# Optimization experiments

Measured on AMD Instinct MI355X. Metric: run time of the kernel, lower is better.

The kernel has to match this reference:

```python
import jax, jax.numpy as jnp
import numpy as np

B, D, AED = 64, 1024, 64
DM = D + AED          # d_model = 1088
H = 8                 # heads, head_dim = 136
DFF = 2048
L = 2                 # encoder layers
R = 487               # reference set size -> total seq = 512
EPS = 1e-5


def setup_inputs() -> dict:
    key = jax.random.key(0)
    ks = jax.random.split(key, 24)
    s = 0.02
    return {
        "query_embedding": jax.random.normal(ks[0], (B, 1, D), jnp.float32),
        "supportActives_embedding": jax.random.normal(ks[1], (B, 12, D), jnp.float32),
        "supportInactives_embedding": jax.random.normal(ks[2], (B, 12, D), jnp.float32),
        "supportSetActivesSize": jax.random.randint(ks[3], (B,), 0, 13, jnp.int64 if jax.config.jax_enable_x64 else jnp.int32),
        "supportSetInactivesSize": jax.random.randint(ks[4], (B,), 0, 13, jnp.int64 if jax.config.jax_enable_x64 else jnp.int32),
        "referenceSet": jax.random.normal(ks[5], (B, R, D), jnp.float32),
        # stacked per-layer params (PyTorch TransformerEncoderLayer, post-norm, relu)
        "Wqkv": jax.random.normal(ks[6], (L, 3 * DM, DM), jnp.float32) * s,
        "bqkv": jnp.zeros((L, 3 * DM), jnp.float32),
        "Wo": jax.random.normal(ks[7], (L, DM, DM), jnp.float32) * s,
        "bo": jnp.zeros((L, DM), jnp.float32),
        "ln1_w": jnp.ones((L, DM), jnp.float32),
        "ln1_b": jnp.zeros((L, DM), jnp.float32),
        "W1": jax.random.normal(ks[8], (L, DFF, DM), jnp.float32) * s,
        "b1": jnp.zeros((L, DFF), jnp.float32),
        "W2": jax.random.normal(ks[9], (L, DM, DFF), jnp.float32) * s,
        "b2": jnp.zeros((L, DM), jnp.float32),
        "ln2_w": jnp.ones((L, DM), jnp.float32),
        "ln2_b": jnp.zeros((L, DM), jnp.float32),
    }


def _ln(x, w, b):
    mu = jnp.mean(x, axis=-1, keepdims=True)
    var = jnp.mean(jnp.square(x - mu), axis=-1, keepdims=True)
    return (x - mu) * jax.lax.rsqrt(var + EPS) * w + b


def _encoder(S, key_pad_mask, Wqkv, bqkv, Wo, bo, ln1_w, ln1_b, W1, b1, W2, b2, ln2_w, ln2_b):
    # key_pad_mask: [B, Sn] bool, True = masked OUT (PyTorch semantics)
    Bn, Sn, _ = S.shape
    hd = DM // H
    bias = jnp.where(key_pad_mask[:, None, None, :], jnp.float32(-1e9), jnp.float32(0.0))
    x = S
    for l in range(L):
        qkv = x @ Wqkv[l].T + bqkv[l]                       # [B,S,3*DM]
        q, k, v = jnp.split(qkv, 3, axis=-1)
        q = q.reshape(Bn, Sn, H, hd)
        k = k.reshape(Bn, Sn, H, hd)
        v = v.reshape(Bn, Sn, H, hd)
        scores = jnp.einsum("bqhd,bkhd->bhqk", q, k) / jnp.sqrt(jnp.float32(hd))
        attn = jax.nn.softmax(scores + bias, axis=-1)
        o = jnp.einsum("bhqk,bkhd->bqhd", attn, v).reshape(Bn, Sn, DM)
        o = o @ Wo[l].T + bo[l]
        x = _ln(x + o, ln1_w[l], ln1_b[l])                  # post-norm
        h = jax.nn.relu(x @ W1[l].T + b1[l])
        x = _ln(x + (h @ W2[l].T + b2[l]), ln2_w[l], ln2_b[l])
    return x


def reference(query_embedding, supportActives_embedding, supportInactives_embedding,
              supportSetActivesSize, supportSetInactivesSize, referenceSet,
              Wqkv, bqkv, Wo, bo, ln1_w, ln1_b, W1, b1, W2, b2, ln2_w, ln2_b):
    Dh = supportActives_embedding.shape[2]
    pad0 = lambda x: jnp.concatenate([x, jnp.zeros_like(x[:, :, :AED])], axis=2)
    q = pad0(query_embedding)
    ref = pad0(referenceSet)
    sa = jnp.concatenate([supportActives_embedding, jnp.ones_like(supportActives_embedding[:, :, :AED])], axis=2)
    si = jnp.concatenate([supportInactives_embedding, -jnp.ones_like(supportInactives_embedding[:, :, :AED])], axis=2)
    S = jnp.concatenate([q, sa, si, ref], axis=1)           # [B, 1+12+12+R, DM]
    Sn = S.shape[1]
    j = jnp.arange(Sn)[None, :]
    ra = supportSetActivesSize[:, None]
    ri = supportSetInactivesSize[:, None]
    # vectorized replica of the double loop; True = mask out (PyTorch semantics)
    mask = (j == 0) | ((j >= 1) & (j < 13) & (j < ra + 1)) | ((j >= 13) & (j < 25) & (j < ri + 13)) | ((j >= 25) & (j < ri + 13))
    S = _encoder(S, mask, Wqkv, bqkv, Wo, bo, ln1_w, ln1_b, W1, b1, W2, b2, ln2_w, ln2_b)
    q_out = S[:, 0:1, :Dh]
    sa_out = S[:, 1:13, :Dh]
    si_out = S[:, 13:25, :Dh]
    return (q_out, sa_out, si_out)
```

## Files before the change

kernel.cpp:

```cpp
#include <hip/hip_runtime.h>

typedef unsigned short u16;
typedef unsigned int u32;
typedef __attribute__((ext_vector_type(8))) short short8;
typedef __attribute__((ext_vector_type(4))) float f32x4;

#define B_ 64
#define D_ 1024
#define DM_ 1088
#define H_ 8
#define HD_ 136
#define DFF_ 2048
#define SN_ 512
#define DM3_ 3264

__device__ __forceinline__ u16 f2bf(float f) {
    union { float f; u32 u; } v; v.f = f;
    u32 r = v.u + 0x7FFFu + ((v.u >> 16) & 1u);
    return (u16)(r >> 16);
}
__device__ __forceinline__ float bf2f(u16 u) {
    union { u32 u; float f; } v; v.u = (u32)u << 16; return v.f;
}

__device__ __forceinline__ void gload16(const void* g, void* l) {
    __builtin_amdgcn_global_load_lds(
        (const __attribute__((address_space(1))) u32*)g,
        (__attribute__((address_space(3))) u32*)l, 16, 0, 0);
}

__global__ void cvt_bf16(const float* __restrict__ in, u16* __restrict__ out, int n) {
    int i = blockIdx.x * 256 + threadIdx.x;
    if (i < n) out[i] = f2bf(in[i]);
}

__global__ void build_s(const float* __restrict__ qe, const float* __restrict__ sa,
                        const float* __restrict__ si, const float* __restrict__ ref,
                        u16* __restrict__ xb) {
    int idx = blockIdx.x * 256 + threadIdx.x;
    const int total = B_ * SN_ * (DM_ / 4);
    if (idx >= total) return;
    int b = idx / (SN_ * 272);
    int rem = idx - b * (SN_ * 272);
    int j = rem / 272;
    int c4 = rem - j * 272;
    int col = c4 * 4;
    float4 v;
    if (col < D_) {
        const float* src;
        if (j == 0)       src = qe + (size_t)b * D_;
        else if (j < 13)  src = sa + ((size_t)b * 12 + (j - 1)) * D_;
        else if (j < 25)  src = si + ((size_t)b * 12 + (j - 13)) * D_;
        else              src = ref + ((size_t)b * 487 + (j - 25)) * D_;
        v = *(const float4*)(src + col);
    } else {
        float f = (j >= 1 && j < 13) ? 1.f : ((j >= 13 && j < 25) ? -1.f : 0.f);
        v = make_float4(f, f, f, f);
    }
    size_t off = ((size_t)b * SN_ + j) * DM_ + col;
    ushort4 p; p.x = f2bf(v.x); p.y = f2bf(v.y); p.z = f2bf(v.z); p.w = f2bf(v.w);
    *(ushort4*)(xb + off) = p;
}

__global__ void build_mask(const int* __restrict__ asz, const int* __restrict__ isz,
                           float* __restrict__ mb) {
    int idx = blockIdx.x * 256 + threadIdx.x;
    if (idx >= B_ * SN_) return;
    int b = idx >> 9, j = idx & 511;
    int ra = asz[b], ri = isz[b];
    bool m = (j == 0) || (j >= 1 && j < 13 && j < ra + 1)
          || (j >= 13 && j < 25 && j < ri + 13) || (j >= 25 && j < ri + 13);
    mb[idx] = m ? -1e9f : 0.f;
}

template<int EPI>
__global__ __launch_bounds__(512, 2)
void gemm256(const u16* __restrict__ A, int lda, const u16* __restrict__ Bt,
             const float* __restrict__ bias, u16* __restrict__ C,
             int N, int K, int nbx) {
    __shared__ __align__(16) u16 As3[3][256 * 32];
    __shared__ __align__(16) u16 Bs3[3][256 * 32];
    const int tid = threadIdx.x;
    const int lane = tid & 63;
    const int l16 = lane & 15;
    const int lhi = lane >> 4;
    const int wave = tid >> 6;
    const int arow = (wave >> 2) * 128;
    const int bcol = (wave & 3) * 64;

    const int nwg = gridDim.x;
    const int cpx = nwg >> 3;
    const int bid = blockIdx.x;
    const int swz = (bid & 7) * cpx + (bid >> 3);
    const int by = swz / nbx;
    const int bx = swz - by * nbx;
    const int bm = by * 256;
    const int bn = bx * 256;

    auto STAGE = [&](int buf, int kt) {
        const int k0 = kt << 5;
        u16* as = As3[buf];
        u16* bs = Bs3[buf];
        #pragma unroll
        for (int p = 0; p < 2; ++p) {
            int c = p * 512 + tid;
            int row = c >> 2;
            int slot = (c & 3) ^ ((row >> 1) & 3);
            gload16(A + (size_t)(bm + row) * lda + k0 + slot * 8, as + c * 8);
            int nr = bn + row; nr = nr < N ? nr : N - 1;
            gload16(Bt + (size_t)nr * K + k0 + slot * 8, bs + c * 8);
        }
    };

    f32x4 acc[8][4] = {};
    const int KT = K >> 5;

    STAGE(0, 0);
    STAGE(1, 1);
    asm volatile("s_waitcnt vmcnt(4)" ::: "memory");
    __builtin_amdgcn_sched_barrier(0);
    __builtin_amdgcn_s_barrier();
    asm volatile("" ::: "memory");

    int buf = 0, buf2 = 2;
    for (int t = 0; t < KT; ++t) {
        const bool more = (t + 2) < KT;
        if (more) STAGE(buf2, t + 2);
        const u16* as = As3[buf];
        const u16* bs = Bs3[buf];
        short8 bfr[4], af[8];
        #pragma unroll
        for (int n = 0; n < 4; ++n) {
            int row = bcol + n * 16 + l16;
            bfr[n] = *(const short8*)&bs[row * 32 + ((lhi ^ ((row >> 1) & 3)) << 3)];
        }
        #pragma unroll
        for (int m = 0; m < 8; ++m) {
            int row = arow + m * 16 + l16;
            af[m] = *(const short8*)&as[row * 32 + ((lhi ^ ((row >> 1) & 3)) << 3)];
        }
        __builtin_amdgcn_s_setprio(1);
        #pragma unroll
        for (int m = 0; m < 8; ++m)
            #pragma unroll
            for (int n = 0; n < 4; ++n)
                acc[m][n] = __builtin_amdgcn_mfma_f32_16x16x32_bf16(af[m], bfr[n], acc[m][n], 0, 0, 0);
        __builtin_amdgcn_s_setprio(0);
        if (t < KT - 1) {
            if (more) asm volatile("s_waitcnt vmcnt(4)" ::: "memory");
            else      asm volatile("s_waitcnt vmcnt(0)" ::: "memory");
            __builtin_amdgcn_sched_barrier(0);
            __builtin_amdgcn_s_barrier();
            asm volatile("" ::: "memory");
        }
        buf = buf == 2 ? 0 : buf + 1;
        buf2 = buf2 == 2 ? 0 : buf2 + 1;
    }

    #pragma unroll
    for (int n = 0; n < 4; ++n) {
        int col = bn + bcol + n * 16 + l16;
        if (col >= N) continue;
        float bv = bias[col];
        #pragma unroll
        for (int m = 0; m < 8; ++m) {
            #pragma unroll
            for (int r = 0; r < 4; ++r) {
                int row = bm + arow + m * 16 + lhi * 4 + r;
                float v = acc[m][n][r] + bv;
                if (EPI == 1) v = v > 0.f ? v : 0.f;
                C[(size_t)row * N + col] = f2bf(v);
            }
        }
    }
}

__global__ __launch_bounds__(256)
void attn_kernel(u16* __restrict__ qkv, const float* __restrict__ maskbias) {
    __shared__ __align__(16) u16 kls[64 * 168];
    __shared__ __align__(16) u16 vts[144 * 72];
    __shared__ __align__(16) u16 pls[4][16 * 72];
    const int qb = blockIdx.x, h = blockIdx.y, b = blockIdx.z;
    const int tid = threadIdx.x;
    const int lane = tid & 63;
    const int l16 = lane & 15;
    const int lhi = lane >> 4;
    const int wave = tid >> 6;

    for (int i = tid; i < 64 * 32; i += 256) { int r = i >> 5, c = 136 + (i & 31); kls[r * 168 + c] = 0; }
    for (int i = tid; i < 8 * 64;  i += 256) { int r = 136 + (i >> 6), c = i & 63; vts[r * 72 + c] = 0; }

    const int q0 = qb * 64 + wave * 16;
    const size_t qrow = ((size_t)b * SN_ + q0 + l16) * DM3_ + (size_t)h * HD_;
    short8 qf[5];
    #pragma unroll
    for (int ks = 0; ks < 5; ++ks) {
        int c0 = ks * 32 + lhi * 8;
        if (c0 < HD_) qf[ks] = *(const short8*)(qkv + qrow + c0);
        else { short8 z = {0,0,0,0,0,0,0,0}; qf[ks] = z; }
    }
    const float inv = 0.08574929257125442f;
    f32x4 o[9] = {};
    float mrun[4], lrun[4];
    #pragma unroll
    for (int r = 0; r < 4; ++r) { mrun[r] = -1e30f; lrun[r] = 0.f; }

    for (int kt = 0; kt < 8; ++kt) {
        __syncthreads();
        const size_t kbase = ((size_t)b * SN_ + kt * 64) * DM3_ + DM_ + (size_t)h * HD_;
        const size_t vbase = kbase + DM_;
        for (int c = tid; c < 64 * 17; c += 256) {
            int r = c / 17, cc = c - r * 17;
            uint4 v = *(const uint4*)(qkv + kbase + (size_t)r * DM3_ + cc * 8);
            *(uint4*)&kls[r * 168 + cc * 8] = v;
        }
        for (int c = tid; c < 64 * 17; c += 256) {
            int r = c & 63, cc = c >> 6;
            uint4 v = *(const uint4*)(qkv + vbase + (size_t)r * DM3_ + cc * 8);
            const u16* pv = (const u16*)&v;
            #pragma unroll
            for (int t = 0; t < 8; ++t) vts[(cc * 8 + t) * 72 + r] = pv[t];
        }
        __syncthreads();

        f32x4 s[4] = {};
        #pragma unroll
        for (int ks = 0; ks < 5; ++ks) {
            #pragma unroll
            for (int n = 0; n < 4; ++n) {
                short8 bfr = *(const short8*)&kls[(n * 16 + l16) * 168 + ks * 32 + lhi * 8];
                s[n] = __builtin_amdgcn_mfma_f32_16x16x32_bf16(qf[ks], bfr, s[n], 0, 0, 0);
            }
        }
        #pragma unroll
        for (int n = 0; n < 4; ++n) {
            float mb = maskbias[b * SN_ + kt * 64 + n * 16 + l16];
            #pragma unroll
            for (int r = 0; r < 4; ++r) s[n][r] = s[n][r] * inv + mb;
        }
        float tmax[4];
        #pragma unroll
        for (int r = 0; r < 4; ++r)
            tmax[r] = fmaxf(fmaxf(s[0][r], s[1][r]), fmaxf(s[2][r], s[3][r]));
        #pragma unroll
        for (int msk = 1; msk <= 8; msk <<= 1)
            #pragma unroll
            for (int r = 0; r < 4; ++r) tmax[r] = fmaxf(tmax[r], __shfl_xor(tmax[r], msk));
        float scale[4];
        #pragma unroll
        for (int r = 0; r < 4; ++r) {
            float mn = fmaxf(mrun[r], tmax[r]);
            scale[r] = __expf(mrun[r] - mn);
            mrun[r] = mn;
        }
        float rs[4] = {0.f, 0.f, 0.f, 0.f};
        u16 pb[4][4];
        #pragma unroll
        for (int n = 0; n < 4; ++n)
            #pragma unroll
            for (int r = 0; r < 4; ++r) {
                float p = __expf(s[n][r] - mrun[r]);
                rs[r] += p;
                pb[n][r] = f2bf(p);
            }
        #pragma unroll
        for (int msk = 1; msk <= 8; msk <<= 1)
            #pragma unroll
            for (int r = 0; r < 4; ++r) rs[r] += __shfl_xor(rs[r], msk);
        #pragma unroll
        for (int r = 0; r < 4; ++r) lrun[r] = lrun[r] * scale[r] + rs[r];
        #pragma unroll
        for (int f = 0; f < 9; ++f)
            #pragma unroll
            for (int r = 0; r < 4; ++r) o[f][r] *= scale[r];
        #pragma unroll
        for (int n = 0; n < 4; ++n)
            #pragma unroll
            for (int r = 0; r < 4; ++r)
                pls[wave][(lhi * 4 + r) * 72 + n * 16 + l16] = pb[n][r];
        #pragma unroll
        for (int ks2 = 0; ks2 < 2; ++ks2) {
            short8 pa = *(const short8*)&pls[wave][l16 * 72 + ks2 * 32 + lhi * 8];
            #pragma unroll
            for (int f = 0; f < 9; ++f) {
                short8 bv = *(const short8*)&vts[(l16 + f * 16) * 72 + ks2 * 32 + lhi * 8];
                o[f] = __builtin_amdgcn_mfma_f32_16x16x32_bf16(pa, bv, o[f], 0, 0, 0);
            }
        }
    }
    #pragma unroll
    for (int f = 0; f < 9; ++f) {
        int d = f * 16 + l16;
        if (d < HD_) {
            #pragma unroll
            for (int r = 0; r < 4; ++r) {
                size_t row = (size_t)b * SN_ + q0 + lhi * 4 + r;
                qkv[row * DM3_ + h * HD_ + d] = f2bf(o[f][r] / lrun[r]);
            }
        }
    }
}

__global__ __launch_bounds__(256)
void add_ln(u16* __restrict__ x, const u16* __restrict__ o,
            const float* __restrict__ w, const float* __restrict__ bb) {
    const int row = blockIdx.x;
    const int tid = threadIdx.x;
    u16* xr = x + (size_t)row * DM_;
    const u16* orr = o + (size_t)row * DM_;
    float v0[4], v1[4];
    float s = 0.f, s2 = 0.f;
    {
        ushort4 a = ((const ushort4*)xr)[tid];
        ushort4 c = ((const ushort4*)orr)[tid];
        v0[0] = bf2f(a.x) + bf2f(c.x); v0[1] = bf2f(a.y) + bf2f(c.y);
        v0[2] = bf2f(a.z) + bf2f(c.z); v0[3] = bf2f(a.w) + bf2f(c.w);
        #pragma unroll
        for (int t = 0; t < 4; ++t) { s += v0[t]; s2 += v0[t] * v0[t]; }
    }
    const bool has2 = tid < 16;
    if (has2) {
        ushort4 a = ((const ushort4*)xr)[256 + tid];
        ushort4 c = ((const ushort4*)orr)[256 + tid];
        v1[0] = bf2f(a.x) + bf2f(c.x); v1[1] = bf2f(a.y) + bf2f(c.y);
        v1[2] = bf2f(a.z) + bf2f(c.z); v1[3] = bf2f(a.w) + bf2f(c.w);
        #pragma unroll
        for (int t = 0; t < 4; ++t) { s += v1[t]; s2 += v1[t] * v1[t]; }
    }
    #pragma unroll
    for (int m = 32; m >= 1; m >>= 1) { s += __shfl_xor(s, m); s2 += __shfl_xor(s2, m); }
    __shared__ float red[8];
    const int wave = tid >> 6, lane = tid & 63;
    if (lane == 0) { red[wave] = s; red[4 + wave] = s2; }
    __syncthreads();
    s = red[0] + red[1] + red[2] + red[3];
    s2 = red[4] + red[5] + red[6] + red[7];
    const float mean = s * (1.f / DM_);
    float var = s2 * (1.f / DM_) - mean * mean;
    const float rstd = rsqrtf(fmaxf(var, 0.f) + 1e-5f);
    {
        float4 wv = ((const float4*)w)[tid], bv = ((const float4*)bb)[tid];
        ushort4 y;
        y.x = f2bf((v0[0] - mean) * rstd * wv.x + bv.x);
        y.y = f2bf((v0[1] - mean) * rstd * wv.y + bv.y);
        y.z = f2bf((v0[2] - mean) * rstd * wv.z + bv.z);
        y.w = f2bf((v0[3] - mean) * rstd * wv.w + bv.w);
        ((ushort4*)xr)[tid] = y;
    }
    if (has2) {
        float4 wv = ((const float4*)w)[256 + tid], bv = ((const float4*)bb)[256 + tid];
        ushort4 y;
        y.x = f2bf((v1[0] - mean) * rstd * wv.x + bv.x);
        y.y = f2bf((v1[1] - mean) * rstd * wv.y + bv.y);
        y.z = f2bf((v1[2] - mean) * rstd * wv.z + bv.z);
        y.w = f2bf((v1[3] - mean) * rstd * wv.w + bv.w);
        ((ushort4*)xr)[256 + tid] = y;
    }
}

__global__ void extract_out(const u16* __restrict__ x, float* __restrict__ out) {
    int idx = blockIdx.x * 256 + threadIdx.x;
    const int total = B_ * 25 * D_;
    if (idx >= total) return;
    int b = idx / (25 * D_);
    int rem = idx - b * 25 * D_;
    int s = rem / D_;
    int c = rem - s * D_;
    float v = bf2f(x[((size_t)b * SN_ + s) * DM_ + c]);
    size_t dst;
    if (s == 0)       dst = (size_t)b * D_ + c;
    else if (s < 13)  dst = (size_t)B_ * D_ + ((size_t)b * 12 + (s - 1)) * D_ + c;
    else              dst = (size_t)B_ * D_ * 13 + ((size_t)b * 12 + (s - 13)) * D_ + c;
    out[dst] = v;
}

extern "C" void kernel_launch(void* const* d_in, const int* in_sizes, int n_in,
                              void* d_out, int out_size, void* d_ws, size_t ws_size,
                              hipStream_t stream) {
    const float* q_emb = (const float*)d_in[0];
    const float* sa_emb = (const float*)d_in[1];
    const float* si_emb = (const float*)d_in[2];
    const int* asz = (const int*)d_in[3];
    const int* isz = (const int*)d_in[4];
    const float* refset = (const float*)d_in[5];
    const float* Wqkv = (const float*)d_in[6];
    const float* bqkv = (const float*)d_in[7];
    const float* Wo = (const float*)d_in[8];
    const float* bo = (const float*)d_in[9];
    const float* ln1w = (const float*)d_in[10];
    const float* ln1b = (const float*)d_in[11];
    const float* W1 = (const float*)d_in[12];
    const float* b1 = (const float*)d_in[13];
    const float* W2 = (const float*)d_in[14];
    const float* b2 = (const float*)d_in[15];
    const float* ln2w = (const float*)d_in[16];
    const float* ln2b = (const float*)d_in[17];

    char* ws = (char*)d_ws;
    auto alloc = [&](size_t bytes) { char* p = ws; ws += (bytes + 255) & ~(size_t)255; return p; };
    const size_t NW_QKV = (size_t)2 * DM3_ * DM_;
    const size_t NW_O = (size_t)2 * DM_ * DM_;
    const size_t NW_1 = (size_t)2 * DFF_ * DM_;
    const size_t NROW = (size_t)B_ * SN_;

    u16* wqkv_b = (u16*)alloc(NW_QKV * 2);
    u16* wo_b   = (u16*)alloc(NW_O * 2);
    u16* w1_b   = (u16*)alloc(NW_1 * 2);
    u16* w2_b   = (u16*)alloc(NW_1 * 2);
    float* mb   = (float*)alloc(NROW * 4);
    u16* xb     = (u16*)alloc(NROW * DM_ * 2);
    u16* qkvb   = (u16*)alloc(NROW * DM3_ * 2);
    u16* ob     = (u16*)alloc(NROW * DM_ * 2);
    u16* bh     = qkvb;

    cvt_bf16<<<(int)((NW_QKV + 255) / 256), 256, 0, stream>>>(Wqkv, wqkv_b, (int)NW_QKV);
    cvt_bf16<<<(int)((NW_O + 255) / 256), 256, 0, stream>>>(Wo, wo_b, (int)NW_O);
    cvt_bf16<<<(int)((NW_1 + 255) / 256), 256, 0, stream>>>(W1, w1_b, (int)NW_1);
    cvt_bf16<<<(int)((NW_1 + 255) / 256), 256, 0, stream>>>(W2, w2_b, (int)NW_1);

    {
        int total = B_ * SN_ * (DM_ / 4);
        build_s<<<(total + 255) / 256, 256, 0, stream>>>(q_emb, sa_emb, si_emb, refset, xb);
        build_mask<<<(B_ * SN_ + 255) / 256, 256, 0, stream>>>(asz, isz, mb);
    }

    const int MB256 = (int)(NROW / 256);
    const int NBX_QKV = (DM3_ + 255) / 256;
    const int NBX_DM  = (DM_ + 255) / 256;
    const int NBX_FF  = DFF_ / 256;
    for (int l = 0; l < 2; ++l) {
        gemm256<0><<<dim3(MB256 * NBX_QKV), 512, 0, stream>>>(
            xb, DM_, wqkv_b + (size_t)l * DM3_ * DM_, bqkv + (size_t)l * DM3_, qkvb, DM3_, DM_, NBX_QKV);
        attn_kernel<<<dim3(8, H_, B_), 256, 0, stream>>>(qkvb, mb);
        gemm256<0><<<dim3(MB256 * NBX_DM), 512, 0, stream>>>(
            qkvb, DM3_, wo_b + (size_t)l * DM_ * DM_, bo + (size_t)l * DM_, ob, DM_, DM_, NBX_DM);
        add_ln<<<(int)NROW, 256, 0, stream>>>(xb, ob, ln1w + (size_t)l * DM_, ln1b + (size_t)l * DM_);
        gemm256<1><<<dim3(MB256 * NBX_FF), 512, 0, stream>>>(
            xb, DM_, w1_b + (size_t)l * DFF_ * DM_, b1 + (size_t)l * DFF_, bh, DFF_, DM_, NBX_FF);
        gemm256<0><<<dim3(MB256 * NBX_DM), 512, 0, stream>>>(
            bh, DFF_, w2_b + (size_t)l * DM_ * DFF_, b2 + (size_t)l * DM_, ob, DM_, DFF_, NBX_DM);
        add_ln<<<(int)NROW, 256, 0, stream>>>(xb, ob, ln2w + (size_t)l * DM_, ln2b + (size_t)l * DM_);
    }

    extract_out<<<(B_ * 25 * D_ + 255) / 256, 256, 0, stream>>>(xb, (float*)d_out);
}
```

Baseline: 3.041 ms.

## Split GEMM k-step into two half-phases and stage epilogue through LDS

The main GEMM loop now splits each k-step into two halves. Each half loads four A fragments, issues part of the next-stage global-to-LDS prefetch (A in the first half, B in the second), and runs sixteen MFMAs. The split spreads memory traffic across the compute and cuts live fragment registers. The epilogue writes bias/ReLU bf16 results into shared memory in 64-row quarters, then stores coalesced 16-byte vectors to global instead of scattered 2-byte stores. In exchange it adds extra barriers per iteration and several syncthreads in the epilogue.

```diff
diff --git a/kernel.cpp b/kernel.cpp
--- a/kernel.cpp
+++ b/kernel.cpp
@@ -120,58 +120,118 @@
     asm volatile("s_waitcnt vmcnt(4)" ::: "memory");
     __builtin_amdgcn_sched_barrier(0);
     __builtin_amdgcn_s_barrier();
-    asm volatile("" ::: "memory");
 
     int buf = 0, buf2 = 2;
     for (int t = 0; t < KT; ++t) {
         const bool more = (t + 2) < KT;
-        if (more) STAGE(buf2, t + 2);
         const u16* as = As3[buf];
         const u16* bs = Bs3[buf];
-        short8 bfr[4], af[8];
+        const int k0n = (t + 2) << 5;
+        short8 af[4], bfr[4];
         #pragma unroll
         for (int n = 0; n < 4; ++n) {
             int row = bcol + n * 16 + l16;
             bfr[n] = *(const short8*)&bs[row * 32 + ((lhi ^ ((row >> 1) & 3)) << 3)];
         }
         #pragma unroll
-        for (int m = 0; m < 8; ++m) {
+        for (int m = 0; m < 4; ++m) {
             int row = arow + m * 16 + l16;
             af[m] = *(const short8*)&as[row * 32 + ((lhi ^ ((row >> 1) & 3)) << 3)];
         }
+        if (more) {
+            u16* dst = As3[buf2];
+            #pragma unroll
+            for (int p = 0; p < 2; ++p) {
+                int c = p * 512 + tid;
+                int row = c >> 2;
+                int slot = (c & 3) ^ ((row >> 1) & 3);
+                gload16(A + (size_t)(bm + row) * lda + k0n + slot * 8, dst + c * 8);
+            }
+        }
+        __builtin_amdgcn_s_barrier();
+        asm volatile("s_waitcnt lgkmcnt(0)" ::: "memory");
+        __builtin_amdgcn_sched_barrier(0);
         __builtin_amdgcn_s_setprio(1);
         #pragma unroll
-        for (int m = 0; m < 8; ++m)
+        for (int m = 0; m < 4; ++m)
             #pragma unroll
             for (int n = 0; n < 4; ++n)
                 acc[m][n] = __builtin_amdgcn_mfma_f32_16x16x32_bf16(af[m], bfr[n], acc[m][n], 0, 0, 0);
+        __builtin_amdgcn_s_setprio(0);
+        __builtin_amdgcn_s_barrier();
+        #pragma unroll
+        for (int m = 0; m < 4; ++m) {
+            int row = arow + 64 + m * 16 + l16;
+            af[m] = *(const short8*)&as[row * 32 + ((lhi ^ ((row >> 1) & 3)) << 3)];
+        }
+        if (more) {
+            u16* dst = Bs3[buf2];
+            #pragma unroll
+            for (int p = 0; p < 2; ++p) {
+                int c = p * 512 + tid;
+                int row = c >> 2;
+                int slot = (c & 3) ^ ((row >> 1) & 3);
+                int nr = bn + row; nr = nr < N ? nr : N - 1;
+                gload16(Bt + (size_t)nr * K + k0n + slot * 8, dst + c * 8);
+            }
+        }
+        __builtin_amdgcn_s_barrier();
+        asm volatile("s_waitcnt lgkmcnt(0)" ::: "memory");
+        __builtin_amdgcn_sched_barrier(0);
+        __builtin_amdgcn_s_setprio(1);
+        #pragma unroll
+        for (int m = 0; m < 4; ++m)
+            #pragma unroll
+            for (int n = 0; n < 4; ++n)
+                acc[4 + m][n] = __builtin_amdgcn_mfma_f32_16x16x32_bf16(af[m], bfr[n], acc[4 + m][n], 0, 0, 0);
         __builtin_amdgcn_s_setprio(0);
         if (t < KT - 1) {
             if (more) asm volatile("s_waitcnt vmcnt(4)" ::: "memory");
             else      asm volatile("s_waitcnt vmcnt(0)" ::: "memory");
             __builtin_amdgcn_sched_barrier(0);
             __builtin_amdgcn_s_barrier();
-            asm volatile("" ::: "memory");
         }
         buf = buf == 2 ? 0 : buf + 1;
         buf2 = buf2 == 2 ? 0 : buf2 + 1;
     }
 
+    __syncthreads();
+    u16* cst = (u16*)As3;
+    const int halfsel = wave >> 2;
     #pragma unroll
-    for (int n = 0; n < 4; ++n) {
-        int col = bn + bcol + n * 16 + l16;
-        if (col >= N) continue;
-        float bv = bias[col];
-        #pragma unroll
-        for (int m = 0; m < 8; ++m) {
-            #pragma unroll
-            for (int r = 0; r < 4; ++r) {
-                int row = bm + arow + m * 16 + lhi * 4 + r;
-                float v = acc[m][n][r] + bv;
-                if (EPI == 1) v = v > 0.f ? v : 0.f;
-                C[(size_t)row * N + col] = f2bf(v);
-            }
-        }
+    for (int qr = 0; qr < 4; ++qr) {
+        if ((qr >> 1) == halfsel) {
+            const int mbase = (qr & 1) * 4;
+            #pragma unroll
+            for (int n = 0; n < 4; ++n) {
+                int col = bcol + n * 16 + l16;
+                int gc = bn + col;
+                float bv = gc < N ? bias[gc] : 0.f;
+                #pragma unroll
+                for (int mm = 0; mm < 4; ++mm) {
+                    int rq = mm * 16 + lhi * 4;
+                    #pragma unroll
+                    for (int r = 0; r < 4; ++r) {
+                        float v = acc[mbase + mm][n][r] + bv;
+                        if (EPI == 1) v = v > 0.f ? v : 0.f;
+                        cst[(rq + r) * 256 + col] = f2bf(v);
+                    }
+                }
+            }
+        }
+        __syncthreads();
+        #pragma unroll
+        for (int i = 0; i < 4; ++i) {
+            int slot = i * 512 + tid;
+            int row = slot >> 5;
+            int chunk = slot & 31;
+            int gc = bn + chunk * 8;
+            if (gc < N) {
+                uint4 v = *(const uint4*)&cst[row * 256 + chunk * 8];
+                *(uint4*)&C[(size_t)(bm + qr * 64 + row) * N + gc] = v;
+            }
+        }
+        __syncthreads();
     }
 }
 
```

After: 2.753 ms. 1.1x faster.
